# Kernel tuning notes

Hardware: AMD Instinct MI355X
Metric: run time of the kernel (lower is better)

The kernel has to match this reference:

```python
import jax, jax.numpy as jnp
import numpy as np

N = 100000   # nodes
E = 1600000  # edges
IN, H1, H2, OUT = 512, 64, 16, 40


def setup_inputs() -> dict:
    key = jax.random.key(0)
    ks = jax.random.split(key, 8)
    x = jax.random.normal(ks[0], (N, IN), jnp.float32)
    edge_index = jax.random.randint(ks[1], (2, E), 0, N, dtype=jnp.int64)

    def glorot(k, i, o):
        s = np.sqrt(6.0 / (i + o)).astype(np.float32)
        return jax.random.uniform(k, (i, o), jnp.float32, -s, s)

    return dict(
        x=x, edge_index=edge_index,
        W1=glorot(ks[2], IN, H1), b1=jnp.zeros((H1,), jnp.float32),
        W2=glorot(ks[3], H1, H2), b2=jnp.zeros((H2,), jnp.float32),
        W3=glorot(ks[4], H2, OUT), b3=jnp.zeros((OUT,), jnp.float32),
    )


def _gcn_conv(x, src, dst, W, b):
    # PyG GCNConv: x' = D^{-1/2} (A + I) D^{-1/2} (x W) + b
    h = x @ W                                   # [N, F_out]
    n = x.shape[0]
    deg = jnp.zeros((n,), h.dtype).at[dst].add(1.0) + 1.0   # self-loop adds 1
    dinv = jax.lax.rsqrt(deg)                   # deg >= 1 always
    norm = dinv[src] * dinv[dst]                # [E]
    msg = h[src] * norm[:, None]                # gather + scale  [E, F_out]
    out = jnp.zeros_like(h).at[dst].add(msg)    # scatter-add to targets
    out = out + h * (dinv * dinv)[:, None]      # self-loop contribution
    return out + b


def reference(x, edge_index, W1, b1, W2, b2, W3, b3):
    src, dst = edge_index[0], edge_index[1]
    h = jax.nn.relu(_gcn_conv(x, src, dst, W1, b1))
    # dropout(p=0.2, training=False) -> identity
    h = jax.nn.relu(_gcn_conv(h, src, dst, W2, b2))
    h = _gcn_conv(h, src, dst, W3, b3)
    return jax.nn.log_softmax(h, axis=-1)
```

## Files before the change

### kernel.cpp

```cpp
#include <hip/hip_runtime.h>
#include <cstdint>
#include <cstddef>

#define NNODES 100000
#define NEDGES 1600000
#define NWIN 100
#define WIN_NODES 1000
#define WCAP 17408
#define WSTR 16

#define GM_ROWS 128
#define APAD 72
#define GEMM_BLOCKS ((NNODES + GM_ROWS - 1) / GM_ROWS)
#define BUCKET_BLOCKS 512
#define BCHUNK ((NEDGES + BUCKET_BLOCKS - 1) / BUCKET_BLOCKS)
#define MEGA_BLOCKS (GEMM_BLOCKS + BUCKET_BLOCKS)

typedef __attribute__((ext_vector_type(8))) short bf16x8;
typedef __attribute__((ext_vector_type(4))) float f32x4;
typedef __attribute__((ext_vector_type(4))) unsigned short ushort4v;
typedef __attribute__((ext_vector_type(8))) unsigned short ushort8v;

__device__ inline unsigned short f2bf(float f) {
    union { float f; unsigned u; } v; v.f = f;
    unsigned r = v.u + 0x7FFFu + ((v.u >> 16) & 1u);
    return (unsigned short)(r >> 16);
}
__device__ inline float bf2f(unsigned short b) {
    union { unsigned u; float f; } v; v.u = ((unsigned)b) << 16; return v.f;
}
__device__ inline void bfpair(unsigned u, float& lo, float& hi) {
    union { unsigned x; float f; } a, b;
    a.x = u << 16; b.x = u & 0xffff0000u;
    lo = a.f; hi = b.f;
}


__global__ __launch_bounds__(256) void convW(const float* __restrict__ W,
                                             unsigned short* __restrict__ Wt,
                                             int* __restrict__ wcur) {
    if (blockIdx.x == 0 && threadIdx.x < NWIN) wcur[threadIdx.x * WSTR] = 0;
    int i = blockIdx.x * 256 + threadIdx.x;
    if (i < 512 * 64) {
        int k = i >> 6, n = i & 63;
        Wt[n * 512 + k] = f2bf(W[i]);
    }
}


__global__ __launch_bounds__(256) void mega_gemm_bucket(
        const float* __restrict__ A,
        const unsigned short* __restrict__ Wt,
        unsigned short* __restrict__ Hs,
        const int* __restrict__ src, const int* __restrict__ dst,
        unsigned* __restrict__ stage,
        int* __restrict__ wcur, int M, int E) {
    __shared__ __align__(16) unsigned char smem[18432 + 9216];

    long long b = blockIdx.x;
    int g0 = (int)((b * GEMM_BLOCKS) / MEGA_BLOCKS);
    int g1 = (int)(((b + 1) * GEMM_BLOCKS) / MEGA_BLOCKS);

    if (g1 > g0) {
        typedef unsigned short RowA[APAD];
        RowA* As = (RowA*)smem;
        RowA* Bs = (RowA*)(smem + 18432);
        const int tid = threadIdx.x;
        const int wid = tid >> 6;
        const int lane = tid & 63;
        const int bm = g0 * GM_ROWS;

        f32x4 acc[2][4];
#pragma unroll
        for (int i = 0; i < 2; i++)
#pragma unroll
            for (int j = 0; j < 4; j++) acc[i][j] = (f32x4){0.f, 0.f, 0.f, 0.f};

        const int ar = tid >> 4;
        const int ac4 = tid & 15;
        const int lm = lane & 15;
        const int lk = (lane >> 4) * 8;

        float4 aR0[8], aR1[8];
        ushort8v bR0[2], bR1[2];

        auto LOADA = [&](float4 (&aRx)[8], ushort8v (&bRx)[2], int k0) {
#pragma unroll
            for (int p = 0; p < 8; p++) {
                int row = bm + p * 16 + ar;
                if (row < M) aRx[p] = *(const float4*)&A[(size_t)row * 512 + k0 + ac4 * 4];
                else         aRx[p] = make_float4(0.f, 0.f, 0.f, 0.f);
            }
#pragma unroll
            for (int p = 0; p < 2; p++) {
                int c = p * 256 + tid;
                int n = c >> 3, kc = c & 7;
                bRx[p] = *(const ushort8v*)&Wt[(size_t)n * 512 + k0 + kc * 8];
            }
        };

        auto TILE = [&](float4 (&aRx)[8], ushort8v (&bRx)[2], int k0) {
#pragma unroll
            for (int p = 0; p < 8; p++) {
                int r = p * 16 + ar;
                unsigned lo, hi;
                asm("v_cvt_pk_bf16_f32 %0, %1, %2" : "=v"(lo) : "v"(aRx[p].x), "v"(aRx[p].y));
                asm("v_cvt_pk_bf16_f32 %0, %1, %2" : "=v"(hi) : "v"(aRx[p].z), "v"(aRx[p].w));
                uint2 u; u.x = lo; u.y = hi;
                *(uint2*)&As[r][ac4 * 4] = u;
            }
#pragma unroll
            for (int p = 0; p < 2; p++) {
                int c = p * 256 + tid;
                int n = c >> 3, kc = c & 7;
                *(ushort8v*)&Bs[n][kc * 8] = bRx[p];
            }
            __syncthreads();

            if (k0 + 128 < 512) LOADA(aRx, bRx, k0 + 128);

            bf16x8 a[2][2], bb[4][2];
#pragma unroll
            for (int rf = 0; rf < 2; rf++)
#pragma unroll
                for (int kf = 0; kf < 2; kf++)
                    a[rf][kf] = *(const bf16x8*)&As[wid * 32 + rf * 16 + lm][kf * 32 + lk];
#pragma unroll
            for (int cf = 0; cf < 4; cf++)
#pragma unroll
                for (int kf = 0; kf < 2; kf++)
                    bb[cf][kf] = *(const bf16x8*)&Bs[cf * 16 + lm][kf * 32 + lk];

            __builtin_amdgcn_s_setprio(1);
#pragma unroll
            for (int kf = 0; kf < 2; kf++)
#pragma unroll
                for (int rf = 0; rf < 2; rf++)
#pragma unroll
                    for (int cf = 0; cf < 4; cf++)
                        acc[rf][cf] = __builtin_amdgcn_mfma_f32_16x16x32_bf16(
                            a[rf][kf], bb[cf][kf], acc[rf][cf], 0, 0, 0);
            __builtin_amdgcn_s_setprio(0);
            __syncthreads();
        };

        LOADA(aR0, bR0, 0);
        LOADA(aR1, bR1, 64);
        for (int tp = 0; tp < 4; tp++) {
            TILE(aR0, bR0, tp * 128);
            TILE(aR1, bR1, tp * 128 + 64);
        }

#pragma unroll
        for (int rf = 0; rf < 2; rf++) {
#pragma unroll
            for (int j = 0; j < 4; j++) {
                int row = bm + wid * 32 + rf * 16 + (lane >> 4) * 4 + j;
                if (row < M) {
#pragma unroll
                    for (int cf = 0; cf < 4; cf++)
                        Hs[(size_t)row * 64 + cf * 16 + lm] = f2bf(acc[rf][cf][j]);
                }
            }
        }
    } else {
        int bi = (int)(b - g0);
        int* cnt  = (int*)smem;
        int* lcur = cnt + NWIN;
        const int tid = threadIdx.x;
        int e0 = bi * BCHUNK;
        int e1 = e0 + BCHUNK; if (e1 > E) e1 = E;

        for (int i = tid; i < NWIN; i += 256) cnt[i] = 0;
        __syncthreads();
        for (int e = e0 + tid; e < e1; e += 256) {
            int d = dst[e];
            atomicAdd(&cnt[d / WIN_NODES], 1);
        }
        __syncthreads();
        for (int i = tid; i < NWIN; i += 256)
            lcur[i] = atomicAdd(&wcur[i * WSTR], cnt[i]);
        __syncthreads();
        for (int e = e0 + tid; e < e1; e += 256) {
            int d = dst[e], s = src[e];
            int w = d / WIN_NODES;
            int pos = atomicAdd(&lcur[w], 1);
            if (pos < WCAP)
                stage[(size_t)w * WCAP + pos] =
                    ((unsigned)(d - w * WIN_NODES) << 17) | (unsigned)s;
        }
    }
}


__global__ __launch_bounds__(256) void csr_window(
        const unsigned* __restrict__ stage,
        const int* __restrict__ wcur,
        int* __restrict__ rowstart,
        float* __restrict__ dinv,
        int* __restrict__ csr,
        unsigned* __restrict__ H32) {
    __shared__ int cnt[WIN_NODES];
    __shared__ float dlds[WIN_NODES];
    __shared__ int red[256];
    const int w = blockIdx.x;
    const int t = threadIdx.x;
    const int wb = w * WIN_NODES;
    const size_t sb = (size_t)w * WCAP;

    int v = (t < w) ? min(wcur[t * WSTR], WCAP) : 0;
    red[t] = v;
    __syncthreads();
#pragma unroll
    for (int off = 128; off > 0; off >>= 1) {
        if (t < off) red[t] += red[t + off];
        __syncthreads();
    }
    int woff = red[0];
    int n_w = min(wcur[w * WSTR], WCAP);
    __syncthreads();

    for (int i = t; i < WIN_NODES; i += 256) cnt[i] = 0;
    __syncthreads();
    for (int i = t; i < n_w; i += 256)
        atomicAdd(&cnt[stage[sb + i] >> 17], 1);
    __syncthreads();

    int c0 = 0, c1 = 0, c2 = 0, c3 = 0, psum = 0;
    if (t < 250) {
        c0 = cnt[4 * t]; c1 = cnt[4 * t + 1]; c2 = cnt[4 * t + 2]; c3 = cnt[4 * t + 3];
        psum = c0 + c1 + c2 + c3;
    }
    red[t] = psum;
    __syncthreads();
#pragma unroll
    for (int off = 1; off < 256; off <<= 1) {
        int tv = (t >= off) ? red[t - off] : 0;
        __syncthreads();
        red[t] += tv;
        __syncthreads();
    }
    int excl = red[t] - psum;
    if (t < 250) {
        int running = woff + excl;
        int idx = 4 * t;
        float d0 = rsqrtf((float)c0 + 1.f), d1 = rsqrtf((float)c1 + 1.f);
        float d2 = rsqrtf((float)c2 + 1.f), d3 = rsqrtf((float)c3 + 1.f);
        rowstart[wb + idx] = running; dinv[wb + idx] = d0; dlds[idx] = d0;
        cnt[idx] = running; running += c0;
        rowstart[wb + idx + 1] = running; dinv[wb + idx + 1] = d1; dlds[idx + 1] = d1;
        cnt[idx + 1] = running; running += c1;
        rowstart[wb + idx + 2] = running; dinv[wb + idx + 2] = d2; dlds[idx + 2] = d2;
        cnt[idx + 2] = running; running += c2;
        rowstart[wb + idx + 3] = running; dinv[wb + idx + 3] = d3; dlds[idx + 3] = d3;
        cnt[idx + 3] = running;
    }
    if (w == NWIN - 1 && t == 0) rowstart[NNODES] = woff + n_w;
    __syncthreads();

    for (int i = t; i < n_w; i += 256) {
        unsigned p = stage[sb + i];
        int dl = (int)(p >> 17);
        int s  = (int)(p & 0x1FFFFu);
        int pos = atomicAdd(&cnt[dl], 1);
        csr[pos] = s;
    }

    for (int i = t; i < WIN_NODES * 32; i += 256) {
        int dl = i >> 5;
        float dd = dlds[dl];
        size_t idx = (size_t)(wb + dl) * 32 + (i & 31);
        unsigned u = H32[idx];
        float lo, hi;
        bfpair(u, lo, hi);
        H32[idx] = (unsigned)f2bf(lo * dd) | ((unsigned)f2bf(hi * dd) << 16);
    }
}


__global__ __launch_bounds__(256) void gather64_l2(
        const int* __restrict__ rowstart, const int* __restrict__ csr,
        const float* __restrict__ dinv,
        const unsigned short* __restrict__ Hs1,
        const float* __restrict__ b1,
        const float* __restrict__ W2,
        unsigned short* __restrict__ Hs2,
        int M) {
    __shared__ float Ws2[64 * 16];
    __shared__ float b1s[64];
    __shared__ float srow[16][68];
    for (int i = threadIdx.x; i < 64 * 16; i += 256) Ws2[i] = W2[i];
    if (threadIdx.x < 64) b1s[threadIdx.x] = b1[threadIdx.x];
    __syncthreads();

    const int r = threadIdx.x >> 4;
    const int lf = threadIdx.x & 15;
    const int row = blockIdx.x * 16 + r;
    const bool rok = (row < M);

    float a0 = 0.f, a1 = 0.f, a2 = 0.f, a3 = 0.f;
    if (rok) {
        const uint2* H8 = (const uint2*)Hs1;
        int e0 = rowstart[row], e1 = rowstart[row + 1];
        uint2 u = H8[(size_t)row * 16 + lf];
        bfpair(u.x, a0, a1); bfpair(u.y, a2, a3);
        int e = e0;
        for (; e + 7 < e1; e += 8) {
            int s0 = csr[e], s1 = csr[e+1], s2 = csr[e+2], s3 = csr[e+3];
            int s4 = csr[e+4], s5 = csr[e+5], s6 = csr[e+6], s7 = csr[e+7];
            uint2 u0 = H8[(size_t)s0 * 16 + lf];
            uint2 u1 = H8[(size_t)s1 * 16 + lf];
            uint2 u2 = H8[(size_t)s2 * 16 + lf];
            uint2 u3 = H8[(size_t)s3 * 16 + lf];
            uint2 u4 = H8[(size_t)s4 * 16 + lf];
            uint2 u5 = H8[(size_t)s5 * 16 + lf];
            uint2 u6 = H8[(size_t)s6 * 16 + lf];
            uint2 u7 = H8[(size_t)s7 * 16 + lf];
            float x0, x1;
            bfpair(u0.x, x0, x1); a0 += x0; a1 += x1; bfpair(u0.y, x0, x1); a2 += x0; a3 += x1;
            bfpair(u1.x, x0, x1); a0 += x0; a1 += x1; bfpair(u1.y, x0, x1); a2 += x0; a3 += x1;
            bfpair(u2.x, x0, x1); a0 += x0; a1 += x1; bfpair(u2.y, x0, x1); a2 += x0; a3 += x1;
            bfpair(u3.x, x0, x1); a0 += x0; a1 += x1; bfpair(u3.y, x0, x1); a2 += x0; a3 += x1;
            bfpair(u4.x, x0, x1); a0 += x0; a1 += x1; bfpair(u4.y, x0, x1); a2 += x0; a3 += x1;
            bfpair(u5.x, x0, x1); a0 += x0; a1 += x1; bfpair(u5.y, x0, x1); a2 += x0; a3 += x1;
            bfpair(u6.x, x0, x1); a0 += x0; a1 += x1; bfpair(u6.y, x0, x1); a2 += x0; a3 += x1;
            bfpair(u7.x, x0, x1); a0 += x0; a1 += x1; bfpair(u7.y, x0, x1); a2 += x0; a3 += x1;
        }
        for (; e < e1; e++) {
            uint2 ue = H8[(size_t)csr[e] * 16 + lf];
            float x0, x1;
            bfpair(ue.x, x0, x1); a0 += x0; a1 += x1;
            bfpair(ue.y, x0, x1); a2 += x0; a3 += x1;
        }
        float dd = dinv[row];
        a0 = fmaxf(a0 * dd + b1s[4 * lf + 0], 0.f);
        a1 = fmaxf(a1 * dd + b1s[4 * lf + 1], 0.f);
        a2 = fmaxf(a2 * dd + b1s[4 * lf + 2], 0.f);
        a3 = fmaxf(a3 * dd + b1s[4 * lf + 3], 0.f);
    }
    float4 t4; t4.x = a0; t4.y = a1; t4.z = a2; t4.w = a3;
    *(float4*)&srow[r][4 * lf] = t4;
    __syncthreads();

    if (rok) {
        float acc = 0.f;
#pragma unroll
        for (int k4 = 0; k4 < 16; k4++) {
            float4 s4 = *(const float4*)&srow[r][k4 * 4];
            acc += s4.x * Ws2[(k4 * 4 + 0) * 16 + lf];
            acc += s4.y * Ws2[(k4 * 4 + 1) * 16 + lf];
            acc += s4.z * Ws2[(k4 * 4 + 2) * 16 + lf];
            acc += s4.w * Ws2[(k4 * 4 + 3) * 16 + lf];
        }
        acc *= dinv[row];
        float hi = __shfl_down(acc, 1, 64);
        if ((lf & 1) == 0) {
            unsigned p = (unsigned)f2bf(acc) | ((unsigned)f2bf(hi) << 16);
            ((unsigned*)Hs2)[(size_t)row * 8 + (lf >> 1)] = p;
        }
    }
}


__global__ __launch_bounds__(256) void gather16_agg(
        const int* __restrict__ rowstart, const int* __restrict__ csr,
        const float* __restrict__ dinv,
        const unsigned short* __restrict__ Hs,
        const float* __restrict__ bias,
        unsigned short* __restrict__ outp,
        int M) {
    __shared__ float bs[16];
    if (threadIdx.x < 16) bs[threadIdx.x] = bias[threadIdx.x];
    __syncthreads();

    const int r = threadIdx.x >> 2;
    const int lf = threadIdx.x & 3;
    const int row = blockIdx.x * 64 + r;
    if (row >= M) return;

    const unsigned long long* H8 = (const unsigned long long*)Hs;
    int e0 = rowstart[row], e1 = rowstart[row + 1];
    unsigned long long u = H8[(size_t)row * 4 + lf];
    float a0, a1, a2, a3;
    bfpair((unsigned)u, a0, a1); bfpair((unsigned)(u >> 32), a2, a3);
    int e = e0;
    for (; e + 7 < e1; e += 8) {
        int s0 = csr[e], s1 = csr[e+1], s2 = csr[e+2], s3 = csr[e+3];
        int s4 = csr[e+4], s5 = csr[e+5], s6 = csr[e+6], s7 = csr[e+7];
        unsigned long long u0 = H8[(size_t)s0 * 4 + lf];
        unsigned long long u1 = H8[(size_t)s1 * 4 + lf];
        unsigned long long u2 = H8[(size_t)s2 * 4 + lf];
        unsigned long long u3 = H8[(size_t)s3 * 4 + lf];
        unsigned long long u4 = H8[(size_t)s4 * 4 + lf];
        unsigned long long u5 = H8[(size_t)s5 * 4 + lf];
        unsigned long long u6 = H8[(size_t)s6 * 4 + lf];
        unsigned long long u7 = H8[(size_t)s7 * 4 + lf];
        float x0, x1;
        bfpair((unsigned)u0, x0, x1); a0 += x0; a1 += x1;
        bfpair((unsigned)(u0 >> 32), x0, x1); a2 += x0; a3 += x1;
        bfpair((unsigned)u1, x0, x1); a0 += x0; a1 += x1;
        bfpair((unsigned)(u1 >> 32), x0, x1); a2 += x0; a3 += x1;
        bfpair((unsigned)u2, x0, x1); a0 += x0; a1 += x1;
        bfpair((unsigned)(u2 >> 32), x0, x1); a2 += x0; a3 += x1;
        bfpair((unsigned)u3, x0, x1); a0 += x0; a1 += x1;
        bfpair((unsigned)(u3 >> 32), x0, x1); a2 += x0; a3 += x1;
        bfpair((unsigned)u4, x0, x1); a0 += x0; a1 += x1;
        bfpair((unsigned)(u4 >> 32), x0, x1); a2 += x0; a3 += x1;
        bfpair((unsigned)u5, x0, x1); a0 += x0; a1 += x1;
        bfpair((unsigned)(u5 >> 32), x0, x1); a2 += x0; a3 += x1;
        bfpair((unsigned)u6, x0, x1); a0 += x0; a1 += x1;
        bfpair((unsigned)(u6 >> 32), x0, x1); a2 += x0; a3 += x1;
        bfpair((unsigned)u7, x0, x1); a0 += x0; a1 += x1;
        bfpair((unsigned)(u7 >> 32), x0, x1); a2 += x0; a3 += x1;
    }
    for (; e < e1; e++) {
        unsigned long long ue = H8[(size_t)csr[e] * 4 + lf];
        float x0, x1;
        bfpair((unsigned)ue, x0, x1); a0 += x0; a1 += x1;
        bfpair((unsigned)(ue >> 32), x0, x1); a2 += x0; a3 += x1;
    }

    float dd = dinv[row];
    a0 = fmaxf(a0 * dd + bs[4 * lf + 0], 0.f) * dd;
    a1 = fmaxf(a1 * dd + bs[4 * lf + 1], 0.f) * dd;
    a2 = fmaxf(a2 * dd + bs[4 * lf + 2], 0.f) * dd;
    a3 = fmaxf(a3 * dd + bs[4 * lf + 3], 0.f) * dd;
    uint2 p;
    p.x = (unsigned)f2bf(a0) | ((unsigned)f2bf(a1) << 16);
    p.y = (unsigned)f2bf(a2) | ((unsigned)f2bf(a3) << 16);
    ((uint2*)outp)[(size_t)row * 4 + lf] = p;
}


__global__ __launch_bounds__(256) void gather16_final(
        const int* __restrict__ rowstart, const int* __restrict__ csr,
        const float* __restrict__ dinv,
        const unsigned short* __restrict__ r2s,
        const float* __restrict__ W3,
        const float* __restrict__ b3,
        float* __restrict__ out,
        int M) {
    __shared__ float Ws3[16 * 40];
    __shared__ float bs3[40];
    __shared__ float srow[64][20];
    __shared__ float orow[64 * 40];
    for (int i = threadIdx.x; i < 16 * 40; i += 256) Ws3[i] = W3[i];
    if (threadIdx.x < 40) bs3[threadIdx.x] = b3[threadIdx.x];

    const int r = threadIdx.x >> 2;
    const int lf = threadIdx.x & 3;
    const int row = blockIdx.x * 64 + r;
    const bool rok = (row < M);

    float a0 = 0.f, a1 = 0.f, a2 = 0.f, a3 = 0.f;
    if (rok) {
        const unsigned long long* H8 = (const unsigned long long*)r2s;
        int e0 = rowstart[row], e1 = rowstart[row + 1];
        unsigned long long u = H8[(size_t)row * 4 + lf];
        bfpair((unsigned)u, a0, a1); bfpair((unsigned)(u >> 32), a2, a3);
        int e = e0;
        for (; e + 7 < e1; e += 8) {
            int s0 = csr[e], s1 = csr[e+1], s2 = csr[e+2], s3 = csr[e+3];
            int s4 = csr[e+4], s5 = csr[e+5], s6 = csr[e+6], s7 = csr[e+7];
            unsigned long long u0 = H8[(size_t)s0 * 4 + lf];
            unsigned long long u1 = H8[(size_t)s1 * 4 + lf];
            unsigned long long u2 = H8[(size_t)s2 * 4 + lf];
            unsigned long long u3 = H8[(size_t)s3 * 4 + lf];
            unsigned long long u4 = H8[(size_t)s4 * 4 + lf];
            unsigned long long u5 = H8[(size_t)s5 * 4 + lf];
            unsigned long long u6 = H8[(size_t)s6 * 4 + lf];
            unsigned long long u7 = H8[(size_t)s7 * 4 + lf];
            float x0, x1;
            bfpair((unsigned)u0, x0, x1); a0 += x0; a1 += x1;
            bfpair((unsigned)(u0 >> 32), x0, x1); a2 += x0; a3 += x1;
            bfpair((unsigned)u1, x0, x1); a0 += x0; a1 += x1;
            bfpair((unsigned)(u1 >> 32), x0, x1); a2 += x0; a3 += x1;
            bfpair((unsigned)u2, x0, x1); a0 += x0; a1 += x1;
            bfpair((unsigned)(u2 >> 32), x0, x1); a2 += x0; a3 += x1;
            bfpair((unsigned)u3, x0, x1); a0 += x0; a1 += x1;
            bfpair((unsigned)(u3 >> 32), x0, x1); a2 += x0; a3 += x1;
            bfpair((unsigned)u4, x0, x1); a0 += x0; a1 += x1;
            bfpair((unsigned)(u4 >> 32), x0, x1); a2 += x0; a3 += x1;
            bfpair((unsigned)u5, x0, x1); a0 += x0; a1 += x1;
            bfpair((unsigned)(u5 >> 32), x0, x1); a2 += x0; a3 += x1;
            bfpair((unsigned)u6, x0, x1); a0 += x0; a1 += x1;
            bfpair((unsigned)(u6 >> 32), x0, x1); a2 += x0; a3 += x1;
            bfpair((unsigned)u7, x0, x1); a0 += x0; a1 += x1;
            bfpair((unsigned)(u7 >> 32), x0, x1); a2 += x0; a3 += x1;
        }
        for (; e < e1; e++) {
            unsigned long long ue = H8[(size_t)csr[e] * 4 + lf];
            float x0, x1;
            bfpair((unsigned)ue, x0, x1); a0 += x0; a1 += x1;
            bfpair((unsigned)(ue >> 32), x0, x1); a2 += x0; a3 += x1;
        }
        float dd = dinv[row];
        a0 *= dd; a1 *= dd; a2 *= dd; a3 *= dd;
    }
    float4 t4; t4.x = a0; t4.y = a1; t4.z = a2; t4.w = a3;
    *(float4*)&srow[r][4 * lf] = t4;
    __syncthreads();

    float vals[10];
#pragma unroll
    for (int q = 0; q < 10; q++) vals[q] = bs3[lf + 4 * q];
#pragma unroll
    for (int k4 = 0; k4 < 4; k4++) {
        float4 s4 = *(const float4*)&srow[r][k4 * 4];
#pragma unroll
        for (int q = 0; q < 10; q++) {
            int n = lf + 4 * q;
            vals[q] += s4.x * Ws3[(k4 * 4 + 0) * 40 + n];
            vals[q] += s4.y * Ws3[(k4 * 4 + 1) * 40 + n];
            vals[q] += s4.z * Ws3[(k4 * 4 + 2) * 40 + n];
            vals[q] += s4.w * Ws3[(k4 * 4 + 3) * 40 + n];
        }
    }
    float m = vals[0];
#pragma unroll
    for (int q = 1; q < 10; q++) m = fmaxf(m, vals[q]);
#pragma unroll
    for (int off = 1; off < 4; off <<= 1) m = fmaxf(m, __shfl_xor(m, off, 64));
    float s = 0.f;
#pragma unroll
    for (int q = 0; q < 10; q++) s += expf(vals[q] - m);
#pragma unroll
    for (int off = 1; off < 4; off <<= 1) s += __shfl_xor(s, off, 64);
    float ls = logf(s) + m;
#pragma unroll
    for (int q = 0; q < 10; q++) orow[r * 40 + lf + 4 * q] = vals[q] - ls;
    __syncthreads();

    float4* o4 = (float4*)(out + (size_t)blockIdx.x * 64 * 40);
    const float4* s4p = (const float4*)orow;
    for (int i = threadIdx.x; i < 640; i += 256) {
        int rr = (i * 4) / 40;
        if (blockIdx.x * 64 + rr < M) o4[i] = s4p[i];
    }
}


extern "C" void kernel_launch(void* const* d_in, const int* in_sizes, int n_in,
                              void* d_out, int out_size, void* d_ws, size_t ws_size,
                              hipStream_t stream) {
    const float* x   = (const float*)d_in[0];
    const int*   ei  = (const int*)d_in[1];
    const int*   src = ei;
    const int*   dst = ei + NEDGES;
    const float* W1 = (const float*)d_in[2];
    const float* b1 = (const float*)d_in[3];
    const float* W2 = (const float*)d_in[4];
    const float* b2 = (const float*)d_in[5];
    const float* W3 = (const float*)d_in[6];
    const float* b3 = (const float*)d_in[7];
    float* out = (float*)d_out;

    int* ws_i = (int*)d_ws;
    int* wcur     = ws_i;
    int* rowstart = wcur + NWIN * WSTR + 16;
    int* csr      = rowstart + NNODES + 8;
    unsigned* stage = (unsigned*)(csr + NEDGES);
    float* dinv   = (float*)(stage + (size_t)NWIN * WCAP);
    unsigned short* Wt = (unsigned short*)(dinv + NNODES);
    float* bufA   = (float*)((int*)(Wt + 64 * 512) + 16);
    float* bufB   = bufA + (size_t)NNODES * 64;

    unsigned short* Hs1 = (unsigned short*)bufA;
    unsigned short* Hs2 = (unsigned short*)bufB;
    unsigned short* r2s = (unsigned short*)bufA;

    convW<<<(512 * 64 + 255) / 256, 256, 0, stream>>>(W1, Wt, wcur);

    mega_gemm_bucket<<<MEGA_BLOCKS, 256, 0, stream>>>(
        x, Wt, Hs1, src, dst, stage, wcur, NNODES, NEDGES);

    csr_window<<<NWIN, 256, 0, stream>>>(stage, wcur, rowstart, dinv, csr,
                                         (unsigned*)Hs1);

    gather64_l2<<<(NNODES + 15) / 16, 256, 0, stream>>>(
        rowstart, csr, dinv, Hs1, b1, W2, Hs2, NNODES);

    gather16_agg<<<(NNODES + 63) / 64, 256, 0, stream>>>(
        rowstart, csr, dinv, Hs2, b2, r2s, NNODES);

    gather16_final<<<(NNODES + 63) / 64, 256, 0, stream>>>(
        rowstart, csr, dinv, r2s, W3, b3, out, NNODES);
}
```

Measured before the change: 209.5 us.

## Fuse GCN pipeline into one persistent cooperative kernel with grid syncs

Replaces the five separate kernel launches (GEMM+bucket, CSR build, three gather layers) with a single persistent cooperative kernel whose phases are separated by grid.sync, with a multi-kernel fallback. The GEMM switches from two register buffers to a single prefetch buffer and drops the setprio hint. The per-node dinv prescale of H1 is moved from the CSR phase into the layer-1 gather, which now multiplies each neighbor by dinv[src]. The aim is to remove launch gaps and tail effects, at the cost of grid-wide barriers, fewer resident blocks (capped at 1024), extra dinv gathers per edge, and a less deeply pipelined GEMM.

Result: slower. 525.8 us (+151.0%).

```diff
diff --git a/kernel.cpp b/kernel.cpp
--- a/kernel.cpp
+++ b/kernel.cpp
@@ -1,6 +1,9 @@
 #include <hip/hip_runtime.h>
+#include <hip/hip_cooperative_groups.h>
 #include <cstdint>
 #include <cstddef>
+
+namespace cg = cooperative_groups;
 
 #define NNODES 100000
 #define NEDGES 1600000
@@ -11,14 +14,11 @@
 
 #define GM_ROWS 128
 #define APAD 72
-#define GEMM_BLOCKS ((NNODES + GM_ROWS - 1) / GM_ROWS)
-#define BUCKET_BLOCKS 512
-#define BCHUNK ((NEDGES + BUCKET_BLOCKS - 1) / BUCKET_BLOCKS)
-#define MEGA_BLOCKS (GEMM_BLOCKS + BUCKET_BLOCKS)
+#define GEMM_TILES ((NNODES + GM_ROWS - 1) / GM_ROWS)
+#define SMEMSZ 27648
 
 typedef __attribute__((ext_vector_type(8))) short bf16x8;
 typedef __attribute__((ext_vector_type(4))) float f32x4;
-typedef __attribute__((ext_vector_type(4))) unsigned short ushort4v;
 typedef __attribute__((ext_vector_type(8))) unsigned short ushort8v;
 
 __device__ inline unsigned short f2bf(float f) {
@@ -26,14 +26,21 @@
     unsigned r = v.u + 0x7FFFu + ((v.u >> 16) & 1u);
     return (unsigned short)(r >> 16);
 }
-__device__ inline float bf2f(unsigned short b) {
-    union { unsigned u; float f; } v; v.u = ((unsigned)b) << 16; return v.f;
-}
 __device__ inline void bfpair(unsigned u, float& lo, float& hi) {
     union { unsigned x; float f; } a, b;
     a.x = u << 16; b.x = u & 0xffff0000u;
     lo = a.f; hi = b.f;
 }
+
+struct GArgs {
+    const float* x; const unsigned short* Wt; unsigned short* Hs1;
+    const int* src; const int* dst; unsigned* stage; int* wcur;
+    int* rowstart; float* dinv; int* csr;
+    const float* b1; const float* W2; unsigned short* Hs2;
+    const float* b2; unsigned short* r2s;
+    const float* W3; const float* b3; float* out;
+    int nbucket;
+};
 
 
 __global__ __launch_bounds__(256) void convW(const float* __restrict__ W,
@@ -48,167 +55,153 @@
 }
 
 
-__global__ __launch_bounds__(256) void mega_gemm_bucket(
-        const float* __restrict__ A,
-        const unsigned short* __restrict__ Wt,
-        unsigned short* __restrict__ Hs,
-        const int* __restrict__ src, const int* __restrict__ dst,
-        unsigned* __restrict__ stage,
-        int* __restrict__ wcur, int M, int E) {
-    __shared__ __align__(16) unsigned char smem[18432 + 9216];
-
-    long long b = blockIdx.x;
-    int g0 = (int)((b * GEMM_BLOCKS) / MEGA_BLOCKS);
-    int g1 = (int)(((b + 1) * GEMM_BLOCKS) / MEGA_BLOCKS);
-
-    if (g1 > g0) {
-        typedef unsigned short RowA[APAD];
-        RowA* As = (RowA*)smem;
-        RowA* Bs = (RowA*)(smem + 18432);
-        const int tid = threadIdx.x;
-        const int wid = tid >> 6;
-        const int lane = tid & 63;
-        const int bm = g0 * GM_ROWS;
-
-        f32x4 acc[2][4];
-#pragma unroll
-        for (int i = 0; i < 2; i++)
-#pragma unroll
-            for (int j = 0; j < 4; j++) acc[i][j] = (f32x4){0.f, 0.f, 0.f, 0.f};
-
-        const int ar = tid >> 4;
-        const int ac4 = tid & 15;
-        const int lm = lane & 15;
-        const int lk = (lane >> 4) * 8;
-
-        float4 aR0[8], aR1[8];
-        ushort8v bR0[2], bR1[2];
-
-        auto LOADA = [&](float4 (&aRx)[8], ushort8v (&bRx)[2], int k0) {
-#pragma unroll
-            for (int p = 0; p < 8; p++) {
-                int row = bm + p * 16 + ar;
-                if (row < M) aRx[p] = *(const float4*)&A[(size_t)row * 512 + k0 + ac4 * 4];
-                else         aRx[p] = make_float4(0.f, 0.f, 0.f, 0.f);
-            }
-#pragma unroll
-            for (int p = 0; p < 2; p++) {
-                int c = p * 256 + tid;
-                int n = c >> 3, kc = c & 7;
-                bRx[p] = *(const ushort8v*)&Wt[(size_t)n * 512 + k0 + kc * 8];
-            }
-        };
-
-        auto TILE = [&](float4 (&aRx)[8], ushort8v (&bRx)[2], int k0) {
-#pragma unroll
-            for (int p = 0; p < 8; p++) {
-                int r = p * 16 + ar;
-                unsigned lo, hi;
-                asm("v_cvt_pk_bf16_f32 %0, %1, %2" : "=v"(lo) : "v"(aRx[p].x), "v"(aRx[p].y));
-                asm("v_cvt_pk_bf16_f32 %0, %1, %2" : "=v"(hi) : "v"(aRx[p].z), "v"(aRx[p].w));
-                uint2 u; u.x = lo; u.y = hi;
-                *(uint2*)&As[r][ac4 * 4] = u;
-            }
-#pragma unroll
-            for (int p = 0; p < 2; p++) {
-                int c = p * 256 + tid;
-                int n = c >> 3, kc = c & 7;
-                *(ushort8v*)&Bs[n][kc * 8] = bRx[p];
-            }
-            __syncthreads();
-
-            if (k0 + 128 < 512) LOADA(aRx, bRx, k0 + 128);
-
-            bf16x8 a[2][2], bb[4][2];
+__device__ __forceinline__ void gemm_tile(const float* __restrict__ A,
+        const unsigned short* __restrict__ Wt, unsigned short* __restrict__ Hs,
+        int g, char* smem) {
+    typedef unsigned short RowA[APAD];
+    RowA* As = (RowA*)smem;
+    RowA* Bs = (RowA*)(smem + 18432);
+    const int tid = threadIdx.x;
+    const int wid = tid >> 6;
+    const int lane = tid & 63;
+    const int bm = g * GM_ROWS;
+
+    f32x4 acc[2][4];
+#pragma unroll
+    for (int i = 0; i < 2; i++)
+#pragma unroll
+        for (int j = 0; j < 4; j++) acc[i][j] = (f32x4){0.f, 0.f, 0.f, 0.f};
+
+    const int ar = tid >> 4;
+    const int ac4 = tid & 15;
+    const int lm = lane & 15;
+    const int lk = (lane >> 4) * 8;
+
+    float4 aR[8];
+    ushort8v bR[2];
+
+    auto LOAD = [&](int k0) {
+#pragma unroll
+        for (int p = 0; p < 8; p++) {
+            int row = bm + p * 16 + ar;
+            if (row < NNODES) aR[p] = *(const float4*)&A[(size_t)row * 512 + k0 + ac4 * 4];
+            else              aR[p] = make_float4(0.f, 0.f, 0.f, 0.f);
+        }
+#pragma unroll
+        for (int p = 0; p < 2; p++) {
+            int c = p * 256 + tid;
+            int n = c >> 3, kc = c & 7;
+            bR[p] = *(const ushort8v*)&Wt[(size_t)n * 512 + k0 + kc * 8];
+        }
+    };
+
+    LOAD(0);
+    for (int k0 = 0; k0 < 512; k0 += 64) {
+#pragma unroll
+        for (int p = 0; p < 8; p++) {
+            int r = p * 16 + ar;
+            unsigned lo, hi;
+            asm("v_cvt_pk_bf16_f32 %0, %1, %2" : "=v"(lo) : "v"(aR[p].x), "v"(aR[p].y));
+            asm("v_cvt_pk_bf16_f32 %0, %1, %2" : "=v"(hi) : "v"(aR[p].z), "v"(aR[p].w));
+            uint2 u; u.x = lo; u.y = hi;
+            *(uint2*)&As[r][ac4 * 4] = u;
+        }
+#pragma unroll
+        for (int p = 0; p < 2; p++) {
+            int c = p * 256 + tid;
+            int n = c >> 3, kc = c & 7;
+            *(ushort8v*)&Bs[n][kc * 8] = bR[p];
+        }
+        __syncthreads();
+
+        if (k0 + 64 < 512) LOAD(k0 + 64);
+
+        bf16x8 af[2][2], bf[4][2];
+#pragma unroll
+        for (int rf = 0; rf < 2; rf++)
+#pragma unroll
+            for (int kf = 0; kf < 2; kf++)
+                af[rf][kf] = *(const bf16x8*)&As[wid * 32 + rf * 16 + lm][kf * 32 + lk];
+#pragma unroll
+        for (int cf = 0; cf < 4; cf++)
+#pragma unroll
+            for (int kf = 0; kf < 2; kf++)
+                bf[cf][kf] = *(const bf16x8*)&Bs[cf * 16 + lm][kf * 32 + lk];
+
+#pragma unroll
+        for (int kf = 0; kf < 2; kf++)
 #pragma unroll
             for (int rf = 0; rf < 2; rf++)
 #pragma unroll
-                for (int kf = 0; kf < 2; kf++)
-                    a[rf][kf] = *(const bf16x8*)&As[wid * 32 + rf * 16 + lm][kf * 32 + lk];
-#pragma unroll
-            for (int cf = 0; cf < 4; cf++)
-#pragma unroll
-                for (int kf = 0; kf < 2; kf++)
-                    bb[cf][kf] = *(const bf16x8*)&Bs[cf * 16 + lm][kf * 32 + lk];
-
-            __builtin_amdgcn_s_setprio(1);
-#pragma unroll
-            for (int kf = 0; kf < 2; kf++)
-#pragma unroll
-                for (int rf = 0; rf < 2; rf++)
-#pragma unroll
-                    for (int cf = 0; cf < 4; cf++)
-                        acc[rf][cf] = __builtin_amdgcn_mfma_f32_16x16x32_bf16(
-                            a[rf][kf], bb[cf][kf], acc[rf][cf], 0, 0, 0);
-            __builtin_amdgcn_s_setprio(0);
-            __syncthreads();
-        };
-
-        LOADA(aR0, bR0, 0);
-        LOADA(aR1, bR1, 64);
-        for (int tp = 0; tp < 4; tp++) {
-            TILE(aR0, bR0, tp * 128);
-            TILE(aR1, bR1, tp * 128 + 64);
-        }
-
-#pragma unroll
-        for (int rf = 0; rf < 2; rf++) {
-#pragma unroll
-            for (int j = 0; j < 4; j++) {
-                int row = bm + wid * 32 + rf * 16 + (lane >> 4) * 4 + j;
-                if (row < M) {
-#pragma unroll
-                    for (int cf = 0; cf < 4; cf++)
-                        Hs[(size_t)row * 64 + cf * 16 + lm] = f2bf(acc[rf][cf][j]);
-                }
-            }
-        }
+                for (int cf = 0; cf < 4; cf++)
+                    acc[rf][cf] = __builtin_amdgcn_mfma_f32_16x16x32_bf16(
+                        af[rf][kf], bf[cf][kf], acc[rf][cf], 0, 0, 0);
+        __syncthreads();
+    }
+
+#pragma unroll
+    for (int rf = 0; rf < 2; rf++) {
+#pragma unroll
+        for (int j = 0; j < 4; j++) {
+            int row = bm + wid * 32 + rf * 16 + (lane >> 4) * 4 + j;
+            if (row < NNODES) {
+#pragma unroll
+                for (int cf = 0; cf < 4; cf++)
+                    Hs[(size_t)row * 64 + cf * 16 + lm] = f2bf(acc[rf][cf][j]);
+            }
+        }
+    }
+}
+
+__device__ __forceinline__ void bucket_chunk(const int* __restrict__ src,
+        const int* __restrict__ dst, unsigned* __restrict__ stage,
+        int* __restrict__ wcur, int e0, int e1, char* smem) {
+    int* cnt  = (int*)smem;
+    int* lcur = cnt + NWIN;
+    const int tid = threadIdx.x;
+    for (int i = tid; i < NWIN; i += 256) cnt[i] = 0;
+    __syncthreads();
+    for (int e = e0 + tid; e < e1; e += 256)
+        atomicAdd(&cnt[dst[e] / WIN_NODES], 1);
+    __syncthreads();
+    for (int i = tid; i < NWIN; i += 256)
+        lcur[i] = atomicAdd(&wcur[i * WSTR], cnt[i]);
+    __syncthreads();
+    for (int e = e0 + tid; e < e1; e += 256) {
+        int d = dst[e], s = src[e];
+        int w = d / WIN_NODES;
+        int pos = atomicAdd(&lcur[w], 1);
+        if (pos < WCAP)
+            stage[(size_t)w * WCAP + pos] =
+                ((unsigned)(d - w * WIN_NODES) << 17) | (unsigned)s;
+    }
+}
+
+__device__ __forceinline__ void phaseA(const GArgs& a, char* smem) {
+    int nb = a.nbucket;
+    int ng = (int)gridDim.x - nb;
+    int bid = (int)blockIdx.x;
+    if (bid < ng) {
+        for (int g = bid; g < GEMM_TILES; g += ng)
+            gemm_tile(a.x, a.Wt, a.Hs1, g, smem);
     } else {
-        int bi = (int)(b - g0);
-        int* cnt  = (int*)smem;
-        int* lcur = cnt + NWIN;
-        const int tid = threadIdx.x;
-        int e0 = bi * BCHUNK;
-        int e1 = e0 + BCHUNK; if (e1 > E) e1 = E;
-
-        for (int i = tid; i < NWIN; i += 256) cnt[i] = 0;
-        __syncthreads();
-        for (int e = e0 + tid; e < e1; e += 256) {
-            int d = dst[e];
-            atomicAdd(&cnt[d / WIN_NODES], 1);
-        }
-        __syncthreads();
-        for (int i = tid; i < NWIN; i += 256)
-            lcur[i] = atomicAdd(&wcur[i * WSTR], cnt[i]);
-        __syncthreads();
-        for (int e = e0 + tid; e < e1; e += 256) {
-            int d = dst[e], s = src[e];
-            int w = d / WIN_NODES;
-            int pos = atomicAdd(&lcur[w], 1);
-            if (pos < WCAP)
-                stage[(size_t)w * WCAP + pos] =
-                    ((unsigned)(d - w * WIN_NODES) << 17) | (unsigned)s;
-        }
-    }
-}
-
-
-__global__ __launch_bounds__(256) void csr_window(
-        const unsigned* __restrict__ stage,
-        const int* __restrict__ wcur,
-        int* __restrict__ rowstart,
-        float* __restrict__ dinv,
-        int* __restrict__ csr,
-        unsigned* __restrict__ H32) {
-    __shared__ int cnt[WIN_NODES];
-    __shared__ float dlds[WIN_NODES];
-    __shared__ int red[256];
-    const int w = blockIdx.x;
+        int bi = bid - ng;
+        int chunk = (NEDGES + nb - 1) / nb;
+        int e0 = bi * chunk;
+        int e1 = e0 + chunk; if (e1 > NEDGES) e1 = NEDGES;
+        bucket_chunk(a.src, a.dst, a.stage, a.wcur, e0, e1, smem);
+    }
+}
+
+
+__device__ __forceinline__ void csr_win(const GArgs& a, int w, char* smem) {
+    int* cnt = (int*)smem;
+    int* red = (int*)(smem + 4096);
     const int t = threadIdx.x;
     const int wb = w * WIN_NODES;
     const size_t sb = (size_t)w * WCAP;
 
-    int v = (t < w) ? min(wcur[t * WSTR], WCAP) : 0;
+    int v = (t < w) ? min(a.wcur[t * WSTR], WCAP) : 0;
     red[t] = v;
     __syncthreads();
 #pragma unroll
@@ -217,13 +210,13 @@
         __syncthreads();
     }
     int woff = red[0];
-    int n_w = min(wcur[w * WSTR], WCAP);
+    int n_w = min(a.wcur[w * WSTR], WCAP);
     __syncthreads();
 
     for (int i = t; i < WIN_NODES; i += 256) cnt[i] = 0;
     __syncthreads();
     for (int i = t; i < n_w; i += 256)
-        atomicAdd(&cnt[stage[sb + i] >> 17], 1);
+        atomicAdd(&cnt[a.stage[sb + i] >> 17], 1);
     __syncthreads();
 
     int c0 = 0, c1 = 0, c2 = 0, c3 = 0, psum = 0;
@@ -244,299 +237,295 @@
     if (t < 250) {
         int running = woff + excl;
         int idx = 4 * t;
-        float d0 = rsqrtf((float)c0 + 1.f), d1 = rsqrtf((float)c1 + 1.f);
-        float d2 = rsqrtf((float)c2 + 1.f), d3 = rsqrtf((float)c3 + 1.f);
-        rowstart[wb + idx] = running; dinv[wb + idx] = d0; dlds[idx] = d0;
+        a.rowstart[wb + idx] = running; a.dinv[wb + idx] = rsqrtf((float)c0 + 1.f);
         cnt[idx] = running; running += c0;
-        rowstart[wb + idx + 1] = running; dinv[wb + idx + 1] = d1; dlds[idx + 1] = d1;
+        a.rowstart[wb + idx + 1] = running; a.dinv[wb + idx + 1] = rsqrtf((float)c1 + 1.f);
         cnt[idx + 1] = running; running += c1;
-        rowstart[wb + idx + 2] = running; dinv[wb + idx + 2] = d2; dlds[idx + 2] = d2;
+        a.rowstart[wb + idx + 2] = running; a.dinv[wb + idx + 2] = rsqrtf((float)c2 + 1.f);
         cnt[idx + 2] = running; running += c2;
-        rowstart[wb + idx + 3] = running; dinv[wb + idx + 3] = d3; dlds[idx + 3] = d3;
+        a.rowstart[wb + idx + 3] = running; a.dinv[wb + idx + 3] = rsqrtf((float)c3 + 1.f);
         cnt[idx + 3] = running;
     }
-    if (w == NWIN - 1 && t == 0) rowstart[NNODES] = woff + n_w;
+    if (w == NWIN - 1 && t == 0) a.rowstart[NNODES] = woff + n_w;
     __syncthreads();
 
     for (int i = t; i < n_w; i += 256) {
-        unsigned p = stage[sb + i];
+        unsigned p = a.stage[sb + i];
         int dl = (int)(p >> 17);
         int s  = (int)(p & 0x1FFFFu);
         int pos = atomicAdd(&cnt[dl], 1);
-        csr[pos] = s;
-    }
-
-    for (int i = t; i < WIN_NODES * 32; i += 256) {
-        int dl = i >> 5;
-        float dd = dlds[dl];
-        size_t idx = (size_t)(wb + dl) * 32 + (i & 31);
-        unsigned u = H32[idx];
-        float lo, hi;
-        bfpair(u, lo, hi);
-        H32[idx] = (unsigned)f2bf(lo * dd) | ((unsigned)f2bf(hi * dd) << 16);
-    }
-}
-
-
-__global__ __launch_bounds__(256) void gather64_l2(
-        const int* __restrict__ rowstart, const int* __restrict__ csr,
-        const float* __restrict__ dinv,
-        const unsigned short* __restrict__ Hs1,
-        const float* __restrict__ b1,
-        const float* __restrict__ W2,
-        unsigned short* __restrict__ Hs2,
-        int M) {
-    __shared__ float Ws2[64 * 16];
-    __shared__ float b1s[64];
-    __shared__ float srow[16][68];
-    for (int i = threadIdx.x; i < 64 * 16; i += 256) Ws2[i] = W2[i];
-    if (threadIdx.x < 64) b1s[threadIdx.x] = b1[threadIdx.x];
+        a.csr[pos] = s;
+    }
+}
+
+__device__ __forceinline__ void phaseB(const GArgs& a, char* smem) {
+    for (int w = blockIdx.x; w < NWIN; w += gridDim.x) csr_win(a, w, smem);
+}
+
+
+__device__ __forceinline__ void phaseC(const GArgs& a, char* smem) {
+    float* Ws2 = (float*)smem;
+    float* b1s = (float*)(smem + 4096);
+    typedef float Row68[68];
+    Row68* srow = (Row68*)(smem + 4352);
+    for (int i = threadIdx.x; i < 64 * 16; i += 256) Ws2[i] = a.W2[i];
+    if (threadIdx.x < 64) b1s[threadIdx.x] = a.b1[threadIdx.x];
     __syncthreads();
 
     const int r = threadIdx.x >> 4;
     const int lf = threadIdx.x & 15;
-    const int row = blockIdx.x * 16 + r;
-    const bool rok = (row < M);
-
-    float a0 = 0.f, a1 = 0.f, a2 = 0.f, a3 = 0.f;
-    if (rok) {
-        const uint2* H8 = (const uint2*)Hs1;
-        int e0 = rowstart[row], e1 = rowstart[row + 1];
-        uint2 u = H8[(size_t)row * 16 + lf];
+    const int ngrp = (NNODES + 15) / 16;
+    const uint2* H8 = (const uint2*)a.Hs1;
+
+    for (int grp = blockIdx.x; grp < ngrp; grp += gridDim.x) {
+        int row = grp * 16 + r;
+        bool rok = (row < NNODES);
+        float a0 = 0.f, a1 = 0.f, a2 = 0.f, a3 = 0.f;
+        float dd = 0.f;
+        if (rok) {
+            int e0 = a.rowstart[row], e1 = a.rowstart[row + 1];
+            dd = a.dinv[row];
+            uint2 u = H8[(size_t)row * 16 + lf];
+            bfpair(u.x, a0, a1); bfpair(u.y, a2, a3);
+            a0 *= dd; a1 *= dd; a2 *= dd; a3 *= dd;
+            int e = e0;
+            for (; e + 3 < e1; e += 4) {
+                int s0 = a.csr[e], s1 = a.csr[e+1], s2 = a.csr[e+2], s3 = a.csr[e+3];
+                float w0 = a.dinv[s0], w1 = a.dinv[s1], w2 = a.dinv[s2], w3 = a.dinv[s3];
+                uint2 u0 = H8[(size_t)s0 * 16 + lf];
+                uint2 u1 = H8[(size_t)s1 * 16 + lf];
+                uint2 u2 = H8[(size_t)s2 * 16 + lf];
+                uint2 u3 = H8[(size_t)s3 * 16 + lf];
+                float x0, x1;
+                bfpair(u0.x, x0, x1); a0 += w0 * x0; a1 += w0 * x1;
+                bfpair(u0.y, x0, x1); a2 += w0 * x0; a3 += w0 * x1;
+                bfpair(u1.x, x0, x1); a0 += w1 * x0; a1 += w1 * x1;
+                bfpair(u1.y, x0, x1); a2 += w1 * x0; a3 += w1 * x1;
+                bfpair(u2.x, x0, x1); a0 += w2 * x0; a1 += w2 * x1;
+                bfpair(u2.y, x0, x1); a2 += w2 * x0; a3 += w2 * x1;
+                bfpair(u3.x, x0, x1); a0 += w3 * x0; a1 += w3 * x1;
+                bfpair(u3.y, x0, x1); a2 += w3 * x0; a3 += w3 * x1;
+            }
+            for (; e < e1; e++) {
+                int s0 = a.csr[e];
+                float w0 = a.dinv[s0];
+                uint2 ue = H8[(size_t)s0 * 16 + lf];
+                float x0, x1;
+                bfpair(ue.x, x0, x1); a0 += w0 * x0; a1 += w0 * x1;
+                bfpair(ue.y, x0, x1); a2 += w0 * x0; a3 += w0 * x1;
+            }
+            a0 = fmaxf(a0 * dd + b1s[4 * lf + 0], 0.f);
+            a1 = fmaxf(a1 * dd + b1s[4 * lf + 1], 0.f);
+            a2 = fmaxf(a2 * dd + b1s[4 * lf + 2], 0.f);
+            a3 = fmaxf(a3 * dd + b1s[4 * lf + 3], 0.f);
+        }
+        float4 t4; t4.x = a0; t4.y = a1; t4.z = a2; t4.w = a3;
+        *(float4*)&srow[r][4 * lf] = t4;
+        __syncthreads();
+
+        if (rok) {
+            float acc = 0.f;
+#pragma unroll
+            for (int k4 = 0; k4 < 16; k4++) {
+                float4 s4 = *(const float4*)&srow[r][k4 * 4];
+                acc += s4.x * Ws2[(k4 * 4 + 0) * 16 + lf];
+                acc += s4.y * Ws2[(k4 * 4 + 1) * 16 + lf];
+                acc += s4.z * Ws2[(k4 * 4 + 2) * 16 + lf];
+                acc += s4.w * Ws2[(k4 * 4 + 3) * 16 + lf];
+            }
+            acc *= dd;
+            float hi = __shfl_down(acc, 1, 64);
+            if ((lf & 1) == 0) {
+                unsigned p = (unsigned)f2bf(acc) | ((unsigned)f2bf(hi) << 16);
+                ((unsigned*)a.Hs2)[(size_t)row * 8 + (lf >> 1)] = p;
+            }
+        }
+        __syncthreads();
+    }
+}
+
+
+__device__ __forceinline__ void phaseD(const GArgs& a, char* smem) {
+    float* bs = (float*)smem;
+    if (threadIdx.x < 16) bs[threadIdx.x] = a.b2[threadIdx.x];
+    __syncthreads();
+
+    const int r = threadIdx.x >> 2;
+    const int lf = threadIdx.x & 3;
+    const int ngrp = (NNODES + 63) / 64;
+    const uint2* H8 = (const uint2*)a.Hs2;
+
+    for (int grp = blockIdx.x; grp < ngrp; grp += gridDim.x) {
+        int row = grp * 64 + r;
+        if (row >= NNODES) continue;
+        int e0 = a.rowstart[row], e1 = a.rowstart[row + 1];
+        uint2 u = H8[(size_t)row * 4 + lf];
+        float a0, a1, a2, a3;
         bfpair(u.x, a0, a1); bfpair(u.y, a2, a3);
         int e = e0;
-        for (; e + 7 < e1; e += 8) {
-            int s0 = csr[e], s1 = csr[e+1], s2 = csr[e+2], s3 = csr[e+3];
-            int s4 = csr[e+4], s5 = csr[e+5], s6 = csr[e+6], s7 = csr[e+7];
-            uint2 u0 = H8[(size_t)s0 * 16 + lf];
-            uint2 u1 = H8[(size_t)s1 * 16 + lf];
-            uint2 u2 = H8[(size_t)s2 * 16 + lf];
-            uint2 u3 = H8[(size_t)s3 * 16 + lf];
-            uint2 u4 = H8[(size_t)s4 * 16 + lf];
-            uint2 u5 = H8[(size_t)s5 * 16 + lf];
-            uint2 u6 = H8[(size_t)s6 * 16 + lf];
-            uint2 u7 = H8[(size_t)s7 * 16 + lf];
+        for (; e + 3 < e1; e += 4) {
+            int s0 = a.csr[e], s1 = a.csr[e+1], s2 = a.csr[e+2], s3 = a.csr[e+3];
+            uint2 u0 = H8[(size_t)s0 * 4 + lf];
+            uint2 u1 = H8[(size_t)s1 * 4 + lf];
+            uint2 u2 = H8[(size_t)s2 * 4 + lf];
+            uint2 u3 = H8[(size_t)s3 * 4 + lf];
             float x0, x1;
-            bfpair(u0.x, x0, x1); a0 += x0; a1 += x1; bfpair(u0.y, x0, x1); a2 += x0; a3 += x1;
-            bfpair(u1.x, x0, x1); a0 += x0; a1 += x1; bfpair(u1.y, x0, x1); a2 += x0; a3 += x1;
-            bfpair(u2.x, x0, x1); a0 += x0; a1 += x1; bfpair(u2.y, x0, x1); a2 += x0; a3 += x1;
-            bfpair(u3.x, x0, x1); a0 += x0; a1 += x1; bfpair(u3.y, x0, x1); a2 += x0; a3 += x1;
-            bfpair(u4.x, x0, x1); a0 += x0; a1 += x1; bfpair(u4.y, x0, x1); a2 += x0; a3 += x1;
-            bfpair(u5.x, x0, x1); a0 += x0; a1 += x1; bfpair(u5.y, x0, x1); a2 += x0; a3 += x1;
-            bfpair(u6.x, x0, x1); a0 += x0; a1 += x1; bfpair(u6.y, x0, x1); a2 += x0; a3 += x1;
-            bfpair(u7.x, x0, x1); a0 += x0; a1 += x1; bfpair(u7.y, x0, x1); a2 += x0; a3 += x1;
+            bfpair(u0.x, x0, x1); a0 += x0; a1 += x1;
+            bfpair(u0.y, x0, x1); a2 += x0; a3 += x1;
+            bfpair(u1.x, x0, x1); a0 += x0; a1 += x1;
+            bfpair(u1.y, x0, x1); a2 += x0; a3 += x1;
+            bfpair(u2.x, x0, x1); a0 += x0; a1 += x1;
+            bfpair(u2.y, x0, x1); a2 += x0; a3 += x1;
+            bfpair(u3.x, x0, x1); a0 += x0; a1 += x1;
+            bfpair(u3.y, x0, x1); a2 += x0; a3 += x1;
         }
         for (; e < e1; e++) {
-            uint2 ue = H8[(size_t)csr[e] * 16 + lf];
+            uint2 ue = H8[(size_t)a.csr[e] * 4 + lf];
             float x0, x1;
             bfpair(ue.x, x0, x1); a0 += x0; a1 += x1;
             bfpair(ue.y, x0, x1); a2 += x0; a3 += x1;
         }
-        float dd = dinv[row];
-        a0 = fmaxf(a0 * dd + b1s[4 * lf + 0], 0.f);
-        a1 = fmaxf(a1 * dd + b1s[4 * lf + 1], 0.f);
-        a2 = fmaxf(a2 * dd + b1s[4 * lf + 2], 0.f);
-        a3 = fmaxf(a3 * dd + b1s[4 * lf + 3], 0.f);
-    }
-    float4 t4; t4.x = a0; t4.y = a1; t4.z = a2; t4.w = a3;
-    *(float4*)&srow[r][4 * lf] = t4;
-    __syncthreads();
-
-    if (rok) {
-        float acc = 0.f;
-#pragma unroll
-        for (int k4 = 0; k4 < 16; k4++) {
-            float4 s4 = *(const float4*)&srow[r][k4 * 4];
-            acc += s4.x * Ws2[(k4 * 4 + 0) * 16 + lf];
-            acc += s4.y * Ws2[(k4 * 4 + 1) * 16 + lf];
-            acc += s4.z * Ws2[(k4 * 4 + 2) * 16 + lf];
-            acc += s4.w * Ws2[(k4 * 4 + 3) * 16 + lf];
-        }
-        acc *= dinv[row];
-        float hi = __shfl_down(acc, 1, 64);
-        if ((lf & 1) == 0) {
-            unsigned p = (unsigned)f2bf(acc) | ((unsigned)f2bf(hi) << 16);
-            ((unsigned*)Hs2)[(size_t)row * 8 + (lf >> 1)] = p;
-        }
-    }
-}
-
-
-__global__ __launch_bounds__(256) void gather16_agg(
-        const int* __restrict__ rowstart, const int* __restrict__ csr,
-        const float* __restrict__ dinv,
-        const unsigned short* __restrict__ Hs,
-        const float* __restrict__ bias,
-        unsigned short* __restrict__ outp,
-        int M) {
-    __shared__ float bs[16];
-    if (threadIdx.x < 16) bs[threadIdx.x] = bias[threadIdx.x];
+        float dd = a.dinv[row];
+        a0 = fmaxf(a0 * dd + bs[4 * lf + 0], 0.f) * dd;
+        a1 = fmaxf(a1 * dd + bs[4 * lf + 1], 0.f) * dd;
+        a2 = fmaxf(a2 * dd + bs[4 * lf + 2], 0.f) * dd;
+        a3 = fmaxf(a3 * dd + bs[4 * lf + 3], 0.f) * dd;
+        uint2 p;
+        p.x = (unsigned)f2bf(a0) | ((unsigned)f2bf(a1) << 16);
+        p.y = (unsigned)f2bf(a2) | ((unsigned)f2bf(a3) << 16);
+        ((uint2*)a.r2s)[(size_t)row * 4 + lf] = p;
+    }
+}
+
+
+__device__ __forceinline__ void phaseE(const GArgs& a, char* smem) {
+    float* Ws3 = (float*)smem;
+    float* bs3 = (float*)(smem + 2560);
+    typedef float Row20[20];
+    Row20* srow = (Row20*)(smem + 2720);
+    float* orow = (float*)(smem + 7840);
+    for (int i = threadIdx.x; i < 16 * 40; i += 256) Ws3[i] = a.W3[i];
+    if (threadIdx.x < 40) bs3[threadIdx.x] = a.b3[threadIdx.x];
     __syncthreads();
 
     const int r = threadIdx.x >> 2;
     const int lf = threadIdx.x & 3;
-    const int row = blockIdx.x * 64 + r;
-    if (row >= M) return;
-
-    const unsigned long long* H8 = (const unsigned long long*)Hs;
-    int e0 = rowstart[row], e1 = rowstart[row + 1];
-    unsigned long long u = H8[(size_t)row * 4 + lf];
-    float a0, a1, a2, a3;
-    bfpair((unsigned)u, a0, a1); bfpair((unsigned)(u >> 32), a2, a3);
-    int e = e0;
-    for (; e + 7 < e1; e += 8) {
-        int s0 = csr[e], s1 = csr[e+1], s2 = csr[e+2], s3 = csr[e+3];
-        int s4 = csr[e+4], s5 = csr[e+5], s6 = csr[e+6], s7 = csr[e+7];
-        unsigned long long u0 = H8[(size_t)s0 * 4 + lf];
-        unsigned long long u1 = H8[(size_t)s1 * 4 + lf];
-        unsigned long long u2 = H8[(size_t)s2 * 4 + lf];
-        unsigned long long u3 = H8[(size_t)s3 * 4 + lf];
-        unsigned long long u4 = H8[(size_t)s4 * 4 + lf];
-        unsigned long long u5 = H8[(size_t)s5 * 4 + lf];
-        unsigned long long u6 = H8[(size_t)s6 * 4 + lf];
-        unsigned long long u7 = H8[(size_t)s7 * 4 + lf];
-        float x0, x1;
-        bfpair((unsigned)u0, x0, x1); a0 += x0; a1 += x1;
-        bfpair((unsigned)(u0 >> 32), x0, x1); a2 += x0; a3 += x1;
-        bfpair((unsigned)u1, x0, x1); a0 += x0; a1 += x1;
-        bfpair((unsigned)(u1 >> 32), x0, x1); a2 += x0; a3 += x1;
-        bfpair((unsigned)u2, x0, x1); a0 += x0; a1 += x1;
-        bfpair((unsigned)(u2 >> 32), x0, x1); a2 += x0; a3 += x1;
-        bfpair((unsigned)u3, x0, x1); a0 += x0; a1 += x1;
-        bfpair((unsigned)(u3 >> 32), x0, x1); a2 += x0; a3 += x1;
-        bfpair((unsigned)u4, x0, x1); a0 += x0; a1 += x1;
-        bfpair((unsigned)(u4 >> 32), x0, x1); a2 += x0; a3 += x1;
-        bfpair((unsigned)u5, x0, x1); a0 += x0; a1 += x1;
-        bfpair((unsigned)(u5 >> 32), x0, x1); a2 += x0; a3 += x1;
-        bfpair((unsigned)u6, x0, x1); a0 += x0; a1 += x1;
-        bfpair((unsigned)(u6 >> 32), x0, x1); a2 += x0; a3 += x1;
-        bfpair((unsigned)u7, x0, x1); a0 += x0; a1 += x1;
-        bfpair((unsigned)(u7 >> 32), x0, x1); a2 += x0; a3 += x1;
-    }
-    for (; e < e1; e++) {
-        unsigned long long ue = H8[(size_t)csr[e] * 4 + lf];
-        float x0, x1;
-        bfpair((unsigned)ue, x0, x1); a0 += x0; a1 += x1;
-        bfpair((unsigned)(ue >> 32), x0, x1); a2 += x0; a3 += x1;
-    }
-
-    float dd = dinv[row];
-    a0 = fmaxf(a0 * dd + bs[4 * lf + 0], 0.f) * dd;
-    a1 = fmaxf(a1 * dd + bs[4 * lf + 1], 0.f) * dd;
-    a2 = fmaxf(a2 * dd + bs[4 * lf + 2], 0.f) * dd;
-    a3 = fmaxf(a3 * dd + bs[4 * lf + 3], 0.f) * dd;
-    uint2 p;
-    p.x = (unsigned)f2bf(a0) | ((unsigned)f2bf(a1) << 16);
-    p.y = (unsigned)f2bf(a2) | ((unsigned)f2bf(a3) << 16);
-    ((uint2*)outp)[(size_t)row * 4 + lf] = p;
-}
-
-
-__global__ __launch_bounds__(256) void gather16_final(
-        const int* __restrict__ rowstart, const int* __restrict__ csr,
-        const float* __restrict__ dinv,
-        const unsigned short* __restrict__ r2s,
-        const float* __restrict__ W3,
-        const float* __restrict__ b3,
-        float* __restrict__ out,
-        int M) {
-    __shared__ float Ws3[16 * 40];
-    __shared__ float bs3[40];
-    __shared__ float srow[64][20];
-    __shared__ float orow[64 * 40];
-    for (int i = threadIdx.x; i < 16 * 40; i += 256) Ws3[i] = W3[i];
-    if (threadIdx.x < 40) bs3[threadIdx.x] = b3[threadIdx.x];
-
-    const int r = threadIdx.x >> 2;
-    const int lf = threadIdx.x & 3;
-    const int row = blockIdx.x * 64 + r;
-    const bool rok = (row < M);
-
-    float a0 = 0.f, a1 = 0.f, a2 = 0.f, a3 = 0.f;
-    if (rok) {
-        const unsigned long long* H8 = (const unsigned long long*)r2s;
-        int e0 = rowstart[row], e1 = rowstart[row + 1];
-        unsigned long long u = H8[(size_t)row * 4 + lf];
-        bfpair((unsigned)u, a0, a1); bfpair((unsigned)(u >> 32), a2, a3);
-        int e = e0;
-        for (; e + 7 < e1; e += 8) {
-            int s0 = csr[e], s1 = csr[e+1], s2 = csr[e+2], s3 = csr[e+3];
-            int s4 = csr[e+4], s5 = csr[e+5], s6 = csr[e+6], s7 = csr[e+7];
-            unsigned long long u0 = H8[(size_t)s0 * 4 + lf];
-            unsigned long long u1 = H8[(size_t)s1 * 4 + lf];
-            unsigned long long u2 = H8[(size_t)s2 * 4 + lf];
-            unsigned long long u3 = H8[(size_t)s3 * 4 + lf];
-            unsigned long long u4 = H8[(size_t)s4 * 4 + lf];
-            unsigned long long u5 = H8[(size_t)s5 * 4 + lf];
-            unsigned long long u6 = H8[(size_t)s6 * 4 + lf];
-            unsigned long long u7 = H8[(size_t)s7 * 4 + lf];
-            float x0, x1;
-            bfpair((unsigned)u0, x0, x1); a0 += x0; a1 += x1;
-            bfpair((unsigned)(u0 >> 32), x0, x1); a2 += x0; a3 += x1;
-            bfpair((unsigned)u1, x0, x1); a0 += x0; a1 += x1;
-            bfpair((unsigned)(u1 >> 32), x0, x1); a2 += x0; a3 += x1;
-            bfpair((unsigned)u2, x0, x1); a0 += x0; a1 += x1;
-            bfpair((unsigned)(u2 >> 32), x0, x1); a2 += x0; a3 += x1;
-            bfpair((unsigned)u3, x0, x1); a0 += x0; a1 += x1;
-            bfpair((unsigned)(u3 >> 32), x0, x1); a2 += x0; a3 += x1;
-            bfpair((unsigned)u4, x0, x1); a0 += x0; a1 += x1;
-            bfpair((unsigned)(u4 >> 32), x0, x1); a2 += x0; a3 += x1;
-            bfpair((unsigned)u5, x0, x1); a0 += x0; a1 += x1;
-            bfpair((unsigned)(u5 >> 32), x0, x1); a2 += x0; a3 += x1;
-            bfpair((unsigned)u6, x0, x1); a0 += x0; a1 += x1;
-            bfpair((unsigned)(u6 >> 32), x0, x1); a2 += x0; a3 += x1;
-            bfpair((unsigned)u7, x0, x1); a0 += x0; a1 += x1;
-            bfpair((unsigned)(u7 >> 32), x0, x1); a2 += x0; a3 += x1;
-        }
-        for (; e < e1; e++) {
-            unsigned long long ue = H8[(size_t)csr[e] * 4 + lf];
-            float x0, x1;
-            bfpair((unsigned)ue, x0, x1); a0 += x0; a1 += x1;
-            bfpair((unsigned)(ue >> 32), x0, x1); a2 += x0; a3 += x1;
-        }
-        float dd = dinv[row];
-        a0 *= dd; a1 *= dd; a2 *= dd; a3 *= dd;
-    }
-    float4 t4; t4.x = a0; t4.y = a1; t4.z = a2; t4.w = a3;
-    *(float4*)&srow[r][4 * lf] = t4;
-    __syncthreads();
-
-    float vals[10];
-#pragma unroll
-    for (int q = 0; q < 10; q++) vals[q] = bs3[lf + 4 * q];
-#pragma unroll
-    for (int k4 = 0; k4 < 4; k4++) {
-        float4 s4 = *(const float4*)&srow[r][k4 * 4];
-#pragma unroll
-        for (int q = 0; q < 10; q++) {
-            int n = lf + 4 * q;
-            vals[q] += s4.x * Ws3[(k4 * 4 + 0) * 40 + n];
-            vals[q] += s4.y * Ws3[(k4 * 4 + 1) * 40 + n];
-            vals[q] += s4.z * Ws3[(k4 * 4 + 2) * 40 + n];
-            vals[q] += s4.w * Ws3[(k4 * 4 + 3) * 40 + n];
-        }
-    }
-    float m = vals[0];
-#pragma unroll
-    for (int q = 1; q < 10; q++) m = fmaxf(m, vals[q]);
-#pragma unroll
-    for (int off = 1; off < 4; off <<= 1) m = fmaxf(m, __shfl_xor(m, off, 64));
-    float s = 0.f;
-#pragma unroll
-    for (int q = 0; q < 10; q++) s += expf(vals[q] - m);
-#pragma unroll
-    for (int off = 1; off < 4; off <<= 1) s += __shfl_xor(s, off, 64);
-    float ls = logf(s) + m;
-#pragma unroll
-    for (int q = 0; q < 10; q++) orow[r * 40 + lf + 4 * q] = vals[q] - ls;
-    __syncthreads();
-
-    float4* o4 = (float4*)(out + (size_t)blockIdx.x * 64 * 40);
-    const float4* s4p = (const float4*)orow;
-    for (int i = threadIdx.x; i < 640; i += 256) {
-        int rr = (i * 4) / 40;
-        if (blockIdx.x * 64 + rr < M) o4[i] = s4p[i];
-    }
+    const int ngrp = (NNODES + 63) / 64;
+    const uint2* H8 = (const uint2*)a.r2s;
+
+    for (int grp = blockIdx.x; grp < ngrp; grp += gridDim.x) {
+        int row = grp * 64 + r;
+        bool rok = (row < NNODES);
+        float a0 = 0.f, a1 = 0.f, a2 = 0.f, a3 = 0.f;
+        if (rok) {
+            int e0 = a.rowstart[row], e1 = a.rowstart[row + 1];
+            uint2 u = H8[(size_t)row * 4 + lf];
+            bfpair(u.x, a0, a1); bfpair(u.y, a2, a3);
+            int e = e0;
+            for (; e + 3 < e1; e += 4) {
+                int s0 = a.csr[e], s1 = a.csr[e+1], s2 = a.csr[e+2], s3 = a.csr[e+3];
+                uint2 u0 = H8[(size_t)s0 * 4 + lf];
+                uint2 u1 = H8[(size_t)s1 * 4 + lf];
+                uint2 u2 = H8[(size_t)s2 * 4 + lf];
+                uint2 u3 = H8[(size_t)s3 * 4 + lf];
+                float x0, x1;
+                bfpair(u0.x, x0, x1); a0 += x0; a1 += x1;
+                bfpair(u0.y, x0, x1); a2 += x0; a3 += x1;
+                bfpair(u1.x, x0, x1); a0 += x0; a1 += x1;
+                bfpair(u1.y, x0, x1); a2 += x0; a3 += x1;
+                bfpair(u2.x, x0, x1); a0 += x0; a1 += x1;
+                bfpair(u2.y, x0, x1); a2 += x0; a3 += x1;
+                bfpair(u3.x, x0, x1); a0 += x0; a1 += x1;
+                bfpair(u3.y, x0, x1); a2 += x0; a3 += x1;
+            }
+            for (; e < e1; e++) {
+                uint2 ue = H8[(size_t)a.csr[e] * 4 + lf];
+                float x0, x1;
+                bfpair(ue.x, x0, x1); a0 += x0; a1 += x1;
+                bfpair(ue.y, x0, x1); a2 += x0; a3 += x1;
+            }
+            float dd = a.dinv[row];
+            a0 *= dd; a1 *= dd; a2 *= dd; a3 *= dd;
+        }
+        float4 t4; t4.x = a0; t4.y = a1; t4.z = a2; t4.w = a3;
+        *(float4*)&srow[r][4 * lf] = t4;
+        __syncthreads();
+
+        float vals[10];
+#pragma unroll
+        for (int q = 0; q < 10; q++) vals[q] = bs3[lf + 4 * q];
+#pragma unroll
+        for (int k4 = 0; k4 < 4; k4++) {
+            float4 s4 = *(const float4*)&srow[r][k4 * 4];
+#pragma unroll
+            for (int q = 0; q < 10; q++) {
+                int n = lf + 4 * q;
+                vals[q] += s4.x * Ws3[(k4 * 4 + 0) * 40 + n];
+                vals[q] += s4.y * Ws3[(k4 * 4 + 1) * 40 + n];
+                vals[q] += s4.z * Ws3[(k4 * 4 + 2) * 40 + n];
+                vals[q] += s4.w * Ws3[(k4 * 4 + 3) * 40 + n];
+            }
+        }
+        float m = vals[0];
+#pragma unroll
+        for (int q = 1; q < 10; q++) m = fmaxf(m, vals[q]);
+#pragma unroll
+        for (int off = 1; off < 4; off <<= 1) m = fmaxf(m, __shfl_xor(m, off, 64));
+        float s = 0.f;
+#pragma unroll
+        for (int q = 0; q < 10; q++) s += expf(vals[q] - m);
+#pragma unroll
+        for (int off = 1; off < 4; off <<= 1) s += __shfl_xor(s, off, 64);
+        float ls = logf(s) + m;
+#pragma unroll
+        for (int q = 0; q < 10; q++) orow[r * 40 + lf + 4 * q] = vals[q] - ls;
+        __syncthreads();
+
+        float4* o4 = (float4*)(a.out + (size_t)grp * 64 * 40);
+        const float4* s4p = (const float4*)orow;
+        for (int i = threadIdx.x; i < 640; i += 256) {
+            int rr = (i * 4) / 40;
+            if (grp * 64 + rr < NNODES) o4[i] = s4p[i];
+        }
+        __syncthreads();
+    }
+}
+
+
+__global__ __launch_bounds__(256, 4) void fused_gcn(GArgs a) {
+    __shared__ __align__(16) char smem[SMEMSZ];
+    cg::grid_group grid = cg::this_grid();
+    phaseA(a, smem);
+    grid.sync();
+    phaseB(a, smem);
+    grid.sync();
+    phaseC(a, smem);
+    grid.sync();
+    phaseD(a, smem);
+    grid.sync();
+    phaseE(a, smem);
+}
+
+
+__global__ __launch_bounds__(256, 4) void kA(GArgs a) {
+    __shared__ __align__(16) char smem[SMEMSZ];
+    phaseA(a, smem);
+}
+__global__ __launch_bounds__(256, 4) void kB(GArgs a) {
+    __shared__ __align__(16) char smem[SMEMSZ];
+    phaseB(a, smem);
+}
+__global__ __launch_bounds__(256, 4) void kC(GArgs a) {
+    __shared__ __align__(16) char smem[SMEMSZ];
+    phaseC(a, smem);
+}
+__global__ __launch_bounds__(256, 4) void kD(GArgs a) {
+    __shared__ __align__(16) char smem[SMEMSZ];
+    phaseD(a, smem);
+}
+__global__ __launch_bounds__(256, 4) void kE(GArgs a) {
+    __shared__ __align__(16) char smem[SMEMSZ];
+    phaseE(a, smem);
 }
 
 
@@ -545,15 +534,12 @@
                               hipStream_t stream) {
     const float* x   = (const float*)d_in[0];
     const int*   ei  = (const int*)d_in[1];
-    const int*   src = ei;
-    const int*   dst = ei + NEDGES;
     const float* W1 = (const float*)d_in[2];
     const float* b1 = (const float*)d_in[3];
     const float* W2 = (const float*)d_in[4];
     const float* b2 = (const float*)d_in[5];
     const float* W3 = (const float*)d_in[6];
     const float* b3 = (const float*)d_in[7];
-    float* out = (float*)d_out;
 
     int* ws_i = (int*)d_ws;
     int* wcur     = ws_i;
@@ -565,24 +551,37 @@
     float* bufA   = (float*)((int*)(Wt + 64 * 512) + 16);
     float* bufB   = bufA + (size_t)NNODES * 64;
 
-    unsigned short* Hs1 = (unsigned short*)bufA;
-    unsigned short* Hs2 = (unsigned short*)bufB;
-    unsigned short* r2s = (unsigned short*)bufA;
-
-    convW<<<(512 * 64 + 255) / 256, 256, 0, stream>>>(W1, Wt, wcur);
-
-    mega_gemm_bucket<<<MEGA_BLOCKS, 256, 0, stream>>>(
-        x, Wt, Hs1, src, dst, stage, wcur, NNODES, NEDGES);
-
-    csr_window<<<NWIN, 256, 0, stream>>>(stage, wcur, rowstart, dinv, csr,
-                                         (unsigned*)Hs1);
-
-    gather64_l2<<<(NNODES + 15) / 16, 256, 0, stream>>>(
-        rowstart, csr, dinv, Hs1, b1, W2, Hs2, NNODES);
-
-    gather16_agg<<<(NNODES + 63) / 64, 256, 0, stream>>>(
-        rowstart, csr, dinv, Hs2, b2, r2s, NNODES);
-
-    gather16_final<<<(NNODES + 63) / 64, 256, 0, stream>>>(
-        rowstart, csr, dinv, r2s, W3, b3, out, NNODES);
-}
+    GArgs a;
+    a.x = x; a.Wt = Wt; a.Hs1 = (unsigned short*)bufA;
+    a.src = ei; a.dst = ei + NEDGES; a.stage = stage; a.wcur = wcur;
+    a.rowstart = rowstart; a.dinv = dinv; a.csr = csr;
+    a.b1 = b1; a.W2 = W2; a.Hs2 = (unsigned short*)bufB;
+    a.b2 = b2; a.r2s = (unsigned short*)bufA;
+    a.W3 = W3; a.b3 = b3; a.out = (float*)d_out;
+
+    convW<<<128, 256, 0, stream>>>(W1, Wt, wcur);
+
+    int maxB = 0;
+    hipError_t qerr = hipOccupancyMaxActiveBlocksPerMultiprocessor(&maxB, fused_gcn, 256, 0);
+
+    hipError_t lerr = hipErrorUnknown;
+    if (qerr == hipSuccess && maxB >= 1) {
+        int grid = maxB * 256;
+        if (grid > 1024) grid = 1024;
+        if (grid >= 256) {
+            a.nbucket = grid / 4;
+            void* params[] = { (void*)&a };
+            lerr = hipLaunchCooperativeKernel((const void*)fused_gcn,
+                                              dim3(grid), dim3(256), params, 0, stream);
+        }
+    }
+
+    if (lerr != hipSuccess) {
+        a.nbucket = 256;
+        kA<<<1024, 256, 0, stream>>>(a);
+        kB<<<NWIN, 256, 0, stream>>>(a);
+        kC<<<(NNODES + 15) / 16, 256, 0, stream>>>(a);
+        kD<<<(NNODES + 63) / 64, 256, 0, stream>>>(a);
+        kE<<<(NNODES + 63) / 64, 256, 0, stream>>>(a);
+    }
+}
```
